# Optimization experiments

Measured on AMD Instinct MI355X. Metric: run time of the kernel, lower is better.

## Reference

```python
import jax, jax.numpy as jnp
import numpy as np

D_MODEL = 1024
MAX_NUM_LAYERS = 4


def setup_inputs() -> dict:
    key = jax.random.key(0)
    ks = jax.random.split(key, 8)
    S, B, D, L = 1024, 2, D_MODEL, 3
    w = lambda k: (jax.random.normal(k, (D, D), dtype=jnp.float32) * 0.02)
    return {
        "x": jax.random.normal(ks[0], (S, B, D), dtype=jnp.float32),
        "layer_outputs": jax.random.normal(ks[1], (L, S, B, D), dtype=jnp.float32),
        "Wq": w(ks[2]), "bq": jnp.zeros((D,), jnp.float32),
        "Wk": w(ks[3]), "bk": jnp.zeros((D,), jnp.float32),
        "Wv": w(ks[4]), "bv": jnp.zeros((D,), jnp.float32),
        "Wo": w(ks[5]), "bo": jnp.zeros((D,), jnp.float32),
        "layer_weights": jnp.ones((MAX_NUM_LAYERS + 1,), jnp.float32),
        "num_heads": 16,
    }


def reference(x, layer_outputs, Wq, bq, Wk, bk, Wv, bv, Wo, bo, layer_weights, num_heads):
    # x: [S, B, D]; layer_outputs: [L, S, B, D] (stacked prev layer outputs)
    S, B, D = x.shape
    H = num_heads
    hd = D // H
    scale = hd ** -0.5
    # q from x only: [S, B*H, hd] -> [BH, S, hd]
    q = (x @ Wq.T + bq).reshape(S, B * H, hd).transpose(1, 0, 2)
    # k/v from x and all previous layer outputs (shared K/V projections)
    xs = jnp.concatenate([x[None], layer_outputs], axis=0)          # [Lp1, S, B, D]
    Lp1 = xs.shape[0]
    k = (xs @ Wk.T + bk).reshape(Lp1, S, B * H, hd).transpose(0, 2, 1, 3)  # [Lp1, BH, S, hd]
    v = (xs @ Wv.T + bv).reshape(Lp1, S, B * H, hd).transpose(0, 2, 1, 3)
    # per-layer scores, softmax over the key axis (torch dim=-2 of stacked scores)
    scores = jnp.einsum('bqd,lbkd->lbqk', q, k) * scale             # [Lp1, BH, S, S]
    attn = jax.nn.softmax(scores, axis=-1)
    lw = jax.nn.softmax(layer_weights[:Lp1])                        # [Lp1]
    combined = jnp.einsum('l,lbqk,lbkd->bqd', lw, attn, v)          # [BH, S, hd]
    combined = combined.transpose(1, 0, 2).reshape(S, B, D)
    return combined @ Wo.T + bo
```

## Files before the change

### kernel.cpp

```cpp
#include <hip/hip_runtime.h>
#include <hip/hip_bf16.h>
#include <math.h>

#define S_LEN   1024
#define BATCH   2
#define DMODEL  1024
#define NHEADS  16
#define HDIM    64
#define BHEADS  32
#define LP1     4
#define ROWS_PL 2048

typedef __attribute__((ext_vector_type(8)))  short bf16x8;
typedef __attribute__((ext_vector_type(4)))  float f32x4;
typedef __attribute__((ext_vector_type(16))) float f32x16;

__device__ inline ushort bf16_rne(float a) {
    unsigned u = __float_as_uint(a);
    return (ushort)((u + 0x7FFFu + ((u >> 16) & 1u)) >> 16);
}
__device__ inline float bf16_up(ushort h) { return __uint_as_float(((unsigned)h) << 16); }
__device__ inline void split_bf16(float a, ushort &hi, ushort &lo) {
    hi = bf16_rne(a);
    lo = bf16_rne(a - bf16_up(hi));
}
__device__ inline uint pk_bf16(float a, float b) {
    float2 f; f.x = a; f.y = b;
    __hip_bfloat162 h = __float22bfloat162_rn(f);
    return *reinterpret_cast<uint*>(&h);
}
#if __has_builtin(__builtin_amdgcn_exp2f)
__device__ inline float fast_exp2(float x) { return __builtin_amdgcn_exp2f(x); }
#else
__device__ inline float fast_exp2(float x) { return exp2f(x); }
#endif

__device__ inline void permswap(uint &a, uint &b) {
    asm("v_permlane32_swap_b32 %0, %1" : "+v"(a), "+v"(b));
}

__device__ inline void glds16(const ushort* g, ushort* l) {
    __builtin_amdgcn_global_load_lds(
        (const __attribute__((address_space(1))) void*)g,
        (__attribute__((address_space(3))) void*)l, 16, 0, 0);
}

__device__ inline void wait4_barrier() {
    asm volatile("s_waitcnt vmcnt(4)" ::: "memory");
    __builtin_amdgcn_s_barrier();
    __builtin_amdgcn_sched_barrier(0);
}
__device__ inline void wait0_barrier() {
    asm volatile("s_waitcnt vmcnt(0)" ::: "memory");
    __builtin_amdgcn_s_barrier();
    __builtin_amdgcn_sched_barrier(0);
}

#define SCLF 0.18033688011112042f

__global__ __launch_bounds__(256)
void presplit(const float* __restrict__ x, const float* __restrict__ lo,
              const float* __restrict__ Wq, const float* __restrict__ Wk,
              const float* __restrict__ Wv, const float* __restrict__ Wo,
              ushort* __restrict__ XsH, ushort* __restrict__ WH,
              ushort* __restrict__ WL)
{
    const int bid = blockIdx.x;
    const float* src; ushort* dh; ushort* dl = nullptr; int local;
    if (bid < 1024)      { src = x;  dh = XsH;           local = bid; }
    else if (bid < 4096) { src = lo; dh = XsH + 2097152; local = bid - 1024; }
    else {
        const int z = (bid - 4096) >> 9;
        local = (bid - 4096) & 511;
        const float* wsrc[4] = { Wq, Wk, Wv, Wo };
        src = wsrc[z];
        dh = WH + (size_t)z * 1048576;
        if (z == 0 || z == 3) dl = WL + (size_t)z * 1048576;
    }
    const int i = (local * 256 + threadIdx.x) * 8;
    float v[8];
    *(float4*)&v[0] = *(const float4*)(src + i);
    *(float4*)&v[4] = *(const float4*)(src + i + 4);
    ushort h[8];
    #pragma unroll
    for (int j = 0; j < 8; ++j) h[j] = bf16_rne(v[j]);
    *(uint4*)(dh + i) = *(uint4*)h;
    if (dl) {
        ushort l[8];
        #pragma unroll
        for (int j = 0; j < 8; ++j) l[j] = bf16_rne(v[j] - bf16_up(h[j]));
        *(uint4*)(dl + i) = *(uint4*)l;
    }
}

__global__ __launch_bounds__(256, 2)
void proj_qkv(const ushort* __restrict__ XsH,
              const ushort* __restrict__ WH, const ushort* __restrict__ WL,
              const float* __restrict__ bq, const float* __restrict__ bk,
              const float* __restrict__ bv,
              ushort* __restrict__ qhb, ushort* __restrict__ qlb,
              ushort* __restrict__ kout, ushort* __restrict__ vout)
{
    __shared__ ushort smem[32768];
    const int bid = blockIdx.x;
    const int t   = threadIdx.x;
    const int wv  = t >> 6, lane = t & 63;
    const int quad = lane >> 4, r = lane & 15;
    const int lrow = lane >> 2;
    const int lch  = ((lane & 3) ^ (lrow & 3) ^ ((lrow >> 2) & 3)) * 8;
    const int q0x  = ((quad ^ (r & 3) ^ ((r >> 2) & 3)) << 3);
    const int cn   = lane & 15;

    if (bid >= 512) {
        const int fid = bid - 512;
        const int xcd = fid & 7, idx = fid >> 3;
        const int mt  = xcd * 2 + (idx >> 4);
        const int nt  = idx & 15;
        const int m0 = mt * 128, n0 = nt * 64;

        const int wm = wv & 1, wn = wv >> 1;
        const int mBase = wm * 64, nBase = wn * 32;

        const ushort* Asrc0 = XsH + (size_t)(m0 + wv * 16 + lrow) * DMODEL + lch;
        const ushort* Asrc1 = Asrc0 + (size_t)64 * DMODEL;
        const ushort* Bhsrc = WH  + (size_t)(n0 + wv * 16 + lrow) * DMODEL + lch;
        const ushort* Blsrc = WL  + (size_t)(n0 + wv * 16 + lrow) * DMODEL + lch;

        f32x4 acc[4][2];
        #pragma unroll
        for (int i = 0; i < 4; ++i)
            #pragma unroll
            for (int j = 0; j < 2; ++j) acc[i][j] = (f32x4){0.f, 0.f, 0.f, 0.f};

        #pragma unroll
        for (int s = 0; s < 2; ++s) {
            ushort* sb = smem + s * 8192;
            const int off = s * 32;
            glds16(Asrc0 + off, sb        + wv * 512);
            glds16(Asrc1 + off, sb + 2048 + wv * 512);
            glds16(Bhsrc + off, sb + 4096 + wv * 512);
            glds16(Blsrc + off, sb + 6144 + wv * 512);
        }

        for (int k = 0; k < 32; ++k) {
            if (k < 31) wait4_barrier(); else wait0_barrier();
            if (k + 2 < 32) {
                ushort* sb = smem + ((k + 2) % 3) * 8192;
                const int off = (k + 2) * 32;
                glds16(Asrc0 + off, sb        + wv * 512);
                glds16(Asrc1 + off, sb + 2048 + wv * 512);
                glds16(Bhsrc + off, sb + 4096 + wv * 512);
                glds16(Blsrc + off, sb + 6144 + wv * 512);
            }
            const ushort* Ah = smem + (k % 3) * 8192;
            const ushort* Bh = Ah + 4096;
            const ushort* Bl = Ah + 6144;
            bf16x8 fa[4], fbh[2], fbl[2];
            #pragma unroll
            for (int i = 0; i < 4; ++i)
                fa[i] = *(const bf16x8*)&Ah[(mBase + i * 16 + r) * 32 + q0x];
            #pragma unroll
            for (int j = 0; j < 2; ++j) {
                fbh[j] = *(const bf16x8*)&Bh[(nBase + j * 16 + r) * 32 + q0x];
                fbl[j] = *(const bf16x8*)&Bl[(nBase + j * 16 + r) * 32 + q0x];
            }
            #pragma unroll
            for (int i = 0; i < 4; ++i)
                #pragma unroll
                for (int j = 0; j < 2; ++j) {
                    acc[i][j] = __builtin_amdgcn_mfma_f32_16x16x32_bf16(fa[i], fbh[j], acc[i][j], 0, 0, 0);
                    acc[i][j] = __builtin_amdgcn_mfma_f32_16x16x32_bf16(fa[i], fbl[j], acc[i][j], 0, 0, 0);
                }
        }

        #pragma unroll
        for (int j = 0; j < 2; ++j) {
            const int n = n0 + nBase + j * 16 + cn;
            const float bvv = bq[n];
            #pragma unroll
            for (int i = 0; i < 4; ++i) {
                const int mrow = m0 + mBase + i * 16 + quad * 4;
                #pragma unroll
                for (int g = 0; g < 4; ++g) {
                    const int m = mrow + g;
                    const float val = (acc[i][j][g] + bvv) * SCLF;
                    const int s = m >> 1, b = m & 1;
                    const int bh = b * 16 + (n >> 6), e = n & 63;
                    const size_t idx2 = (((size_t)bh * S_LEN) + s) * HDIM + e;
                    ushort hi, lov; split_bf16(val, hi, lov);
                    qhb[idx2] = hi; qlb[idx2] = lov;
                }
            }
        }
    } else {
        const int xcd = bid & 7, idx = bid >> 3;
        const int mt  = xcd * 8 + (idx >> 3);
        const int nt  = idx & 7;
        const int m0 = mt * 128, n0 = nt * 128;
        const int lyr = m0 >> 11;

        const int wm = wv & 1, wn = wv >> 1;
        const int mBase = wm * 64, nBase = wn * 64;

        const ushort* KWh = WH + 1048576;
        const ushort* VWh = WH + 2097152;
        const ushort* Asrc0 = XsH + (size_t)(m0 + wv * 16 + lrow) * DMODEL + lch;
        const ushort* Asrc1 = Asrc0 + (size_t)64 * DMODEL;
        const ushort* Bw[2] = { KWh, VWh };
        const ushort* Bsrc[2][2];
        #pragma unroll
        for (int p = 0; p < 2; ++p)
            #pragma unroll
            for (int seg = 0; seg < 2; ++seg)
                Bsrc[p][seg] = Bw[p] + (size_t)(n0 + wv * 32 + seg * 16 + lrow) * DMODEL + lch;

        f32x4 aK[4][4], aV[4][4];
        #pragma unroll
        for (int i = 0; i < 4; ++i)
            #pragma unroll
            for (int j = 0; j < 4; ++j) {
                aK[i][j] = (f32x4){0.f, 0.f, 0.f, 0.f};
                aV[i][j] = (f32x4){0.f, 0.f, 0.f, 0.f};
            }

        {
            ushort* ab = smem;
            glds16(Asrc0, ab        + wv * 512);
            glds16(Asrc1, ab + 2048 + wv * 512);
            #pragma unroll
            for (int s = 0; s < 2; ++s) {
                ushort* bb = smem + 8192 + s * 8192;
                const int off = s * 32;
                #pragma unroll
                for (int p = 0; p < 2; ++p)
                    #pragma unroll
                    for (int seg = 0; seg < 2; ++seg)
                        glds16(Bsrc[p][seg] + off, bb + p * 4096 + (wv * 2 + seg) * 512);
            }
        }

        for (int k = 0; k < 32; ++k) {
            if (k < 31) wait4_barrier(); else wait0_barrier();
            if (k + 1 < 32) {
                ushort* ab = smem + ((k + 1) & 1) * 4096;
                const int off = (k + 1) * 32;
                glds16(Asrc0 + off, ab        + wv * 512);
                glds16(Asrc1 + off, ab + 2048 + wv * 512);
            }
            if (k + 2 < 32) {
                ushort* bb = smem + 8192 + ((k + 2) % 3) * 8192;
                const int off = (k + 2) * 32;
                #pragma unroll
                for (int p = 0; p < 2; ++p)
                    #pragma unroll
                    for (int seg = 0; seg < 2; ++seg)
                        glds16(Bsrc[p][seg] + off, bb + p * 4096 + (wv * 2 + seg) * 512);
            }
            const ushort* Ah = smem + (k & 1) * 4096;
            const ushort* Bb = smem + 8192 + (k % 3) * 8192;

            bf16x8 fa[4];
            #pragma unroll
            for (int i = 0; i < 4; ++i)
                fa[i] = *(const bf16x8*)&Ah[(mBase + i * 16 + r) * 32 + q0x];
            #pragma unroll
            for (int j = 0; j < 4; ++j) {
                const int off2 = (nBase + j * 16 + r) * 32 + q0x;
                const bf16x8 fkh = *(const bf16x8*)&Bb[off2];
                const bf16x8 fvh = *(const bf16x8*)&Bb[4096 + off2];
                #pragma unroll
                for (int i = 0; i < 4; ++i) {
                    aK[i][j] = __builtin_amdgcn_mfma_f32_16x16x32_bf16(fa[i], fkh, aK[i][j], 0, 0, 0);
                    aV[i][j] = __builtin_amdgcn_mfma_f32_16x16x32_bf16(fa[i], fvh, aV[i][j], 0, 0, 0);
                }
            }
        }

        #pragma unroll
        for (int j = 0; j < 4; ++j) {
            const int n = n0 + nBase + j * 16 + cn;
            const float bb = bk[n];
            const int e    = n & 63;
            const int es_k = e >> 4, half_k = (e >> 3) & 1, j_k = e & 7;
            const int h    = n >> 6;
            #pragma unroll
            for (int i = 0; i < 4; ++i) {
                #pragma unroll
                for (int g = 0; g < 4; ++g) {
                    const int m = m0 + mBase + i * 16 + quad * 4 + g;
                    const int rem = m & 2047, s = rem >> 1, b = rem & 1;
                    const int bhI = lyr * 32 + b * 16 + h;
                    const int kt  = s >> 5;
                    const int lnk = half_k * 32 + (s & 31);
                    kout[(size_t)bhI * 65536 + (size_t)(kt * 4 + es_k) * 512 + lnk * 8 + j_k]
                        = bf16_rne(aK[i][j][g] + bb);
                }
            }
        }

        ushort* T = smem;
        __syncthreads();
        #pragma unroll
        for (int j = 0; j < 4; ++j) {
            const int nloc = nBase + j * 16 + cn;
            const float bb = bv[n0 + nloc];
            #pragma unroll
            for (int i = 0; i < 4; ++i) {
                #pragma unroll
                for (int g = 0; g < 4; ++g) {
                    const int mloc = mBase + i * 16 + quad * 4 + g;
                    T[nloc * 130 + mloc] = bf16_rne(aV[i][j][g] + bb);
                }
            }
        }
        __syncthreads();
        {
            const int nloc = t >> 1, bsel = t & 1;
            const int n = n0 + nloc, h = n >> 6;
            const int e = n & 63;
            const int dg = e >> 5, lid_v = e & 31;
            const int s0g = (m0 & 2047) >> 1;
            const int kt0 = s0g >> 5;
            const int bhI = lyr * 32 + bsel * 16 + h;
            #pragma unroll
            for (int c = 0; c < 8; ++c) {
                ushort tmp[8];
                #pragma unroll
                for (int j = 0; j < 8; ++j)
                    tmp[j] = T[nloc * 130 + 2 * (c * 8 + j) + bsel];
                const int kt = kt0 + (c >> 2);
                const int c2 = c & 3;
                const int ks = c2 >> 1, hv = c2 & 1;
                ushort* dstb = vout + (size_t)bhI * 65536 + (size_t)kt * 2048;
                *(uint4*)(dstb + (ks * 2 + dg) * 512 + (hv * 32 + lid_v) * 8) = *(uint4*)tmp;
            }
        }
    }
}

__global__ __launch_bounds__(256)
void proj_o(const ushort* __restrict__ Abf,
            const ushort* __restrict__ Bhg, const ushort* __restrict__ Blg,
            const float* __restrict__ bias, float* __restrict__ outf)
{
    __shared__ ushort smem[3][8192];

    const int fid = blockIdx.x;
    const int xcd = fid & 7, idx = fid >> 3;
    const int mt  = xcd * 2 + (idx >> 4);
    const int nt  = idx & 15;
    const int m0 = mt * 128, n0 = nt * 64;

    const int t  = threadIdx.x;
    const int wv = t >> 6, lane = t & 63;
    const int quad = lane >> 4, r = lane & 15;
    const int wm = wv & 1, wn = wv >> 1;
    const int mBase = wm * 64, nBase = wn * 32;

    const int lrow = lane >> 2;
    const int lch  = ((lane & 3) ^ (lrow & 3) ^ ((lrow >> 2) & 3)) * 8;
    const ushort* Asrc0 = Abf + (size_t)(m0 + wv * 16 + lrow) * DMODEL + lch;
    const ushort* Asrc1 = Asrc0 + (size_t)64 * DMODEL;
    const ushort* Bhsrc = Bhg + (size_t)(n0 + wv * 16 + lrow) * DMODEL + lch;
    const ushort* Blsrc = Blg + (size_t)(n0 + wv * 16 + lrow) * DMODEL + lch;

    const int q0x = ((quad ^ (r & 3) ^ ((r >> 2) & 3)) << 3);
    f32x4 acc[4][2];
    #pragma unroll
    for (int i = 0; i < 4; ++i)
        #pragma unroll
        for (int j = 0; j < 2; ++j) acc[i][j] = (f32x4){0.f, 0.f, 0.f, 0.f};

    #pragma unroll
    for (int s = 0; s < 2; ++s) {
        ushort* sb = smem[s];
        const int off = s * 32;
        glds16(Asrc0 + off, sb        + wv * 512);
        glds16(Asrc1 + off, sb + 2048 + wv * 512);
        glds16(Bhsrc + off, sb + 4096 + wv * 512);
        glds16(Blsrc + off, sb + 6144 + wv * 512);
    }

    for (int k = 0; k < 32; ++k) {
        if (k < 31) wait4_barrier(); else wait0_barrier();
        if (k + 2 < 32) {
            ushort* sb = smem[(k + 2) % 3];
            const int off = (k + 2) * 32;
            glds16(Asrc0 + off, sb        + wv * 512);
            glds16(Asrc1 + off, sb + 2048 + wv * 512);
            glds16(Bhsrc + off, sb + 4096 + wv * 512);
            glds16(Blsrc + off, sb + 6144 + wv * 512);
        }
        const ushort* Ah = smem[k % 3];
        const ushort* Bh = Ah + 4096;
        const ushort* Bl = Ah + 6144;
        bf16x8 fa[4], fbh[2], fbl[2];
        #pragma unroll
        for (int i = 0; i < 4; ++i)
            fa[i] = *(const bf16x8*)&Ah[(mBase + i * 16 + r) * 32 + q0x];
        #pragma unroll
        for (int j = 0; j < 2; ++j) {
            fbh[j] = *(const bf16x8*)&Bh[(nBase + j * 16 + r) * 32 + q0x];
            fbl[j] = *(const bf16x8*)&Bl[(nBase + j * 16 + r) * 32 + q0x];
        }
        #pragma unroll
        for (int i = 0; i < 4; ++i)
            #pragma unroll
            for (int j = 0; j < 2; ++j) {
                acc[i][j] = __builtin_amdgcn_mfma_f32_16x16x32_bf16(fa[i], fbh[j], acc[i][j], 0, 0, 0);
                acc[i][j] = __builtin_amdgcn_mfma_f32_16x16x32_bf16(fa[i], fbl[j], acc[i][j], 0, 0, 0);
            }
    }

    const int cn = lane & 15;
    #pragma unroll
    for (int j = 0; j < 2; ++j) {
        const int n = n0 + nBase + j * 16 + cn;
        const float bvv = bias[n];
        #pragma unroll
        for (int i = 0; i < 4; ++i) {
            const int mrow = m0 + mBase + i * 16 + quad * 4;
            #pragma unroll
            for (int g = 0; g < 4; ++g)
                outf[(size_t)(mrow + g) * DMODEL + n] = acc[i][j][g] + bvv;
        }
    }
}

__global__ __launch_bounds__(256, 2)
void attn_mfma(const ushort* __restrict__ qhg, const ushort* __restrict__ qlg,
               const ushort* __restrict__ kh, const ushort* __restrict__ vth,
               const float* __restrict__ lwraw, float* __restrict__ part)
{
    const int t    = threadIdx.x;
    const int wv   = t >> 6, lane = t & 63;
    const int half = lane >> 5, lid = lane & 31;

    const int fid  = blockIdx.x;
    const int xcd  = fid & 7, slot = fid >> 3;
    const int pair = xcd * 16 + (slot >> 2);
    const int qt   = slot & 3;
    const int bh   = pair & 31, l = pair >> 5;
    const int qbase = qt * 256 + wv * 64;

    float wl;
    {
        float v[LP1], wm = -3.0e38f;
        #pragma unroll
        for (int i = 0; i < LP1; ++i) { v[i] = lwraw[i]; wm = fmaxf(wm, v[i]); }
        float ws = 0.f;
        #pragma unroll
        for (int i = 0; i < LP1; ++i) { v[i] = __expf(v[i] - wm); ws += v[i]; }
        wl = v[l] / ws;
    }

    bf16x8 qh[2][4], ql[2][4];
    #pragma unroll
    for (int u = 0; u < 2; ++u) {
        const size_t qoff = ((size_t)bh * S_LEN + qbase + u * 32 + lid) * HDIM + half * 8;
        #pragma unroll
        for (int es = 0; es < 4; ++es) {
            qh[u][es] = *(const bf16x8*)(qhg + qoff + es * 16);
            ql[u][es] = *(const bf16x8*)(qlg + qoff + es * 16);
        }
    }

    f32x16 o[2][2];
    #pragma unroll
    for (int u = 0; u < 2; ++u)
        #pragma unroll
        for (int dg = 0; dg < 2; ++dg)
            #pragma unroll
            for (int i = 0; i < 16; ++i) o[u][dg][i] = 0.f;
    float ls[2] = {0.f, 0.f};

    f32x16 zf;
    #pragma unroll
    for (int i = 0; i < 16; ++i) zf[i] = 0.f;

    const size_t kvo = (size_t)(l * BHEADS + bh) * S_LEN * HDIM;
    const ushort* kfb = kh  + kvo + (size_t)lane * 8;
    const ushort* vfb = vth + kvo + (size_t)lane * 8;

    bf16x8 kb[4], kn[4];
    #pragma unroll
    for (int es = 0; es < 4; ++es)
        kb[es] = *(const bf16x8*)(kfb + es * 512);
    #pragma unroll
    for (int es = 0; es < 4; ++es)
        kn[es] = *(const bf16x8*)(kfb + 2048 + es * 512);

    f32x16 sa[2];
    #pragma unroll
    for (int es = 0; es < 4; ++es)
        #pragma unroll
        for (int u = 0; u < 2; ++u) {
            sa[u] = __builtin_amdgcn_mfma_f32_32x32x16_bf16(kb[es], qh[u][es],
                                                            es == 0 ? zf : sa[u], 0, 0, 0);
            sa[u] = __builtin_amdgcn_mfma_f32_32x32x16_bf16(kb[es], ql[u][es], sa[u], 0, 0, 0);
        }

    for (int kt = 0; kt < 32; ++kt) {
        bf16x8 vb[2][2];
        {
            const ushort* vp = vfb + (size_t)kt * 2048;
            #pragma unroll
            for (int ks = 0; ks < 2; ++ks)
                #pragma unroll
                for (int dg = 0; dg < 2; ++dg)
                    vb[ks][dg] = *(const bf16x8*)(vp + (ks * 2 + dg) * 512);
        }

        bf16x8 pf[2][2];
        #pragma unroll
        for (int ks = 0; ks < 2; ++ks) {
            #pragma unroll
            for (int u = 0; u < 2; ++u) {
                const float p0 = fast_exp2(sa[u][8 * ks + 0]);
                const float p1 = fast_exp2(sa[u][8 * ks + 1]);
                const float p2 = fast_exp2(sa[u][8 * ks + 2]);
                const float p3 = fast_exp2(sa[u][8 * ks + 3]);
                const float p4 = fast_exp2(sa[u][8 * ks + 4]);
                const float p5 = fast_exp2(sa[u][8 * ks + 5]);
                const float p6 = fast_exp2(sa[u][8 * ks + 6]);
                const float p7 = fast_exp2(sa[u][8 * ks + 7]);
                ls[u] += ((p0 + p1) + (p2 + p3)) + ((p4 + p5) + (p6 + p7));

                uint a0 = pk_bf16(p0, p1);
                uint a1 = pk_bf16(p2, p3);
                uint b0 = pk_bf16(p4, p5);
                uint b1 = pk_bf16(p6, p7);
                permswap(a0, b0);
                permswap(a1, b1);
                union { uint w[4]; bf16x8 v; } pu;
                pu.w[0] = a0; pu.w[1] = a1; pu.w[2] = b0; pu.w[3] = b1;
                pf[ks][u] = pu.v;
            }
        }

        #pragma unroll
        for (int es = 0; es < 4; ++es) kb[es] = kn[es];
        {
            const ushort* kp = kfb + (size_t)((kt + 2) & 31) * 2048;
            #pragma unroll
            for (int es = 0; es < 4; ++es) kn[es] = *(const bf16x8*)(kp + es * 512);
        }

        __builtin_amdgcn_s_setprio(1);
        #pragma unroll
        for (int es = 0; es < 4; ++es)
            #pragma unroll
            for (int u = 0; u < 2; ++u) {
                sa[u] = __builtin_amdgcn_mfma_f32_32x32x16_bf16(kb[es], qh[u][es],
                                                                es == 0 ? zf : sa[u], 0, 0, 0);
                sa[u] = __builtin_amdgcn_mfma_f32_32x32x16_bf16(kb[es], ql[u][es], sa[u], 0, 0, 0);
            }
        __builtin_amdgcn_s_setprio(0);

        __builtin_amdgcn_s_setprio(1);
        #pragma unroll
        for (int ks = 0; ks < 2; ++ks)
            #pragma unroll
            for (int dg = 0; dg < 2; ++dg)
                #pragma unroll
                for (int u = 0; u < 2; ++u)
                    o[u][dg] = __builtin_amdgcn_mfma_f32_32x32x16_bf16(vb[ks][dg], pf[ks][u], o[u][dg], 0, 0, 0);
        __builtin_amdgcn_s_setprio(0);
    }

    const int b = bh >> 4, hh = bh & 15;
    #pragma unroll
    for (int u = 0; u < 2; ++u) {
        float lsv = ls[u];
        lsv += __shfl_xor(lsv, 32);
        const float sc = wl / lsv;
        const int q = qbase + u * 32 + lid;
        float* pb = part + (size_t)l * (ROWS_PL * DMODEL)
                  + ((size_t)q * BATCH + b) * DMODEL + hh * HDIM;
        #pragma unroll
        for (int dg = 0; dg < 2; ++dg)
            #pragma unroll
            for (int rq = 0; rq < 4; ++rq) {
                float4 vv;
                vv.x = o[u][dg][rq * 4 + 0] * sc;
                vv.y = o[u][dg][rq * 4 + 1] * sc;
                vv.z = o[u][dg][rq * 4 + 2] * sc;
                vv.w = o[u][dg][rq * 4 + 3] * sc;
                *(float4*)(pb + dg * 32 + rq * 8 + half * 4) = vv;
            }
    }
}

__global__ __launch_bounds__(256)
void sum_y(const float* __restrict__ part, ushort* __restrict__ YH)
{
    const int i = (blockIdx.x * 256 + threadIdx.x) * 8;
    float acc[8];
    #pragma unroll
    for (int c = 0; c < 2; ++c) {
        float4 s = *(const float4*)(part + i + c * 4);
        #pragma unroll
        for (int l = 1; l < LP1; ++l) {
            const float4 p = *(const float4*)(part + (size_t)l * 2097152 + i + c * 4);
            s.x += p.x; s.y += p.y; s.z += p.z; s.w += p.w;
        }
        acc[c * 4 + 0] = s.x; acc[c * 4 + 1] = s.y;
        acc[c * 4 + 2] = s.z; acc[c * 4 + 3] = s.w;
    }
    uint out[4];
    #pragma unroll
    for (int c = 0; c < 4; ++c) out[c] = pk_bf16(acc[c * 2], acc[c * 2 + 1]);
    *(uint4*)(YH + i) = *(uint4*)out;
}

extern "C" void kernel_launch(void* const* d_in, const int* in_sizes, int n_in,
                              void* d_out, int out_size, void* d_ws, size_t ws_size,
                              hipStream_t stream) {
    const float* x  = (const float*)d_in[0];
    const float* lo = (const float*)d_in[1];
    const float* Wq = (const float*)d_in[2];
    const float* bq = (const float*)d_in[3];
    const float* Wk = (const float*)d_in[4];
    const float* bk = (const float*)d_in[5];
    const float* Wv = (const float*)d_in[6];
    const float* bv = (const float*)d_in[7];
    const float* Wo = (const float*)d_in[8];
    const float* bo = (const float*)d_in[9];
    const float* lw = (const float*)d_in[10];
    float* out = (float*)d_out;

    char* ws = (char*)d_ws;
    ushort* XsH  = (ushort*)(ws);
    ushort* WH   = (ushort*)(ws + 16777216);
    ushort* WL   = (ushort*)(ws + 25165824);
    ushort* qhb  = (ushort*)(ws + 33554432);
    ushort* qlb  = (ushort*)(ws + 37748736);
    ushort* khb  = (ushort*)(ws + 41943040);
    ushort* vthb = (ushort*)(ws + 58720256);
    float*  part = (float*)(ws + 75497472);
    ushort* YH   = (ushort*)(ws + 109051904);

    dim3 blk(256);
    presplit<<<dim3(6144), blk, 0, stream>>>(x, lo, Wq, Wk, Wv, Wo, XsH, WH, WL);
    proj_qkv<<<dim3(768), blk, 0, stream>>>(XsH, WH, WL, bq, bk, bv,
                                            qhb, qlb, khb, vthb);
    attn_mfma<<<dim3(512), blk, 0, stream>>>(qhb, qlb, khb, vthb, lw, part);
    sum_y<<<dim3(1024), blk, 0, stream>>>(part, YH);
    proj_o<<<dim3(256), blk, 0, stream>>>(YH, WH + 3145728, WL + 3145728, bo, out);
}
```

Before: 231.8 us.

## Fuse per-layer partial sum into output projection A-tile loading

Removes the separate sum_y kernel and has the output projection read the four fp32 per-layer partial buffers directly. It sums and converts them to bf16 in registers before writing the A tile to shared memory. The B-tile pipeline shrinks from triple to double buffering, with register prefetch of the next A chunk overlapping the MFMA work. This drops one launch and the bf16 intermediate round trip. In exchange each proj_o block rereads 4x fp32 A data (16 column tiles share the same rows), which adds global traffic and register pressure.

```diff
diff --git a/kernel.cpp b/kernel.cpp
--- a/kernel.cpp
+++ b/kernel.cpp
@@ -339,11 +339,11 @@
 }
 
 __global__ __launch_bounds__(256)
-void proj_o(const ushort* __restrict__ Abf,
-            const ushort* __restrict__ Bhg, const ushort* __restrict__ Blg,
-            const float* __restrict__ bias, float* __restrict__ outf)
+void proj_oy(const float* __restrict__ part,
+             const ushort* __restrict__ Bhg, const ushort* __restrict__ Blg,
+             const float* __restrict__ bias, float* __restrict__ outf)
 {
-    __shared__ ushort smem[3][8192];
+    __shared__ ushort smem[2][8192];
 
     const int fid = blockIdx.x;
     const int xcd = fid & 7, idx = fid >> 3;
@@ -359,10 +359,12 @@
 
     const int lrow = lane >> 2;
     const int lch  = ((lane & 3) ^ (lrow & 3) ^ ((lrow >> 2) & 3)) * 8;
-    const ushort* Asrc0 = Abf + (size_t)(m0 + wv * 16 + lrow) * DMODEL + lch;
-    const ushort* Asrc1 = Asrc0 + (size_t)64 * DMODEL;
+    const float* Ap0 = part + (size_t)(m0 + wv * 16 + lrow) * DMODEL + lch;
+    const float* Ap1 = Ap0 + (size_t)64 * DMODEL;
     const ushort* Bhsrc = Bhg + (size_t)(n0 + wv * 16 + lrow) * DMODEL + lch;
     const ushort* Blsrc = Blg + (size_t)(n0 + wv * 16 + lrow) * DMODEL + lch;
+    const int aoff0 = wv * 512 + lane * 8;
+    const int aoff1 = 2048 + wv * 512 + lane * 8;
 
     const int q0x = ((quad ^ (r & 3) ^ ((r >> 2) & 3)) << 3);
     f32x4 acc[4][2];
@@ -371,27 +373,50 @@
         #pragma unroll
         for (int j = 0; j < 2; ++j) acc[i][j] = (f32x4){0.f, 0.f, 0.f, 0.f};
 
-    #pragma unroll
-    for (int s = 0; s < 2; ++s) {
-        ushort* sb = smem[s];
-        const int off = s * 32;
-        glds16(Asrc0 + off, sb        + wv * 512);
-        glds16(Asrc1 + off, sb + 2048 + wv * 512);
-        glds16(Bhsrc + off, sb + 4096 + wv * 512);
-        glds16(Blsrc + off, sb + 6144 + wv * 512);
+    auto sum_cvt = [&](const float* ap, uint4* outv) {
+        float4 s0 = *(const float4*)(ap);
+        float4 s1 = *(const float4*)(ap + 4);
+        #pragma unroll
+        for (int l = 1; l < LP1; ++l) {
+            const float4 p0 = *(const float4*)(ap + (size_t)l * 2097152);
+            const float4 p1 = *(const float4*)(ap + (size_t)l * 2097152 + 4);
+            s0.x += p0.x; s0.y += p0.y; s0.z += p0.z; s0.w += p0.w;
+            s1.x += p1.x; s1.y += p1.y; s1.z += p1.z; s1.w += p1.w;
+        }
+        ushort h[8];
+        h[0] = bf16_rne(s0.x); h[1] = bf16_rne(s0.y);
+        h[2] = bf16_rne(s0.z); h[3] = bf16_rne(s0.w);
+        h[4] = bf16_rne(s1.x); h[5] = bf16_rne(s1.y);
+        h[6] = bf16_rne(s1.z); h[7] = bf16_rne(s1.w);
+        *outv = *(const uint4*)h;
+    };
+
+    {
+        uint4 a0, a1;
+        sum_cvt(Ap0, &a0);
+        sum_cvt(Ap1, &a1);
+        glds16(Bhsrc, smem[0] + 4096 + wv * 512);
+        glds16(Blsrc, smem[0] + 6144 + wv * 512);
+        *(uint4*)&smem[0][aoff0] = a0;
+        *(uint4*)&smem[0][aoff1] = a1;
     }
 
     for (int k = 0; k < 32; ++k) {
-        if (k < 31) wait4_barrier(); else wait0_barrier();
-        if (k + 2 < 32) {
-            ushort* sb = smem[(k + 2) % 3];
-            const int off = (k + 2) * 32;
-            glds16(Asrc0 + off, sb        + wv * 512);
-            glds16(Asrc1 + off, sb + 2048 + wv * 512);
-            glds16(Bhsrc + off, sb + 4096 + wv * 512);
-            glds16(Blsrc + off, sb + 6144 + wv * 512);
-        }
-        const ushort* Ah = smem[k % 3];
+        __syncthreads();
+        float4 ar[2][LP1][2];
+        if (k + 1 < 32) {
+            const int off = (k + 1) * 32;
+            #pragma unroll
+            for (int l = 0; l < LP1; ++l) {
+                ar[0][l][0] = *(const float4*)(Ap0 + (size_t)l * 2097152 + off);
+                ar[0][l][1] = *(const float4*)(Ap0 + (size_t)l * 2097152 + off + 4);
+                ar[1][l][0] = *(const float4*)(Ap1 + (size_t)l * 2097152 + off);
+                ar[1][l][1] = *(const float4*)(Ap1 + (size_t)l * 2097152 + off + 4);
+            }
+            glds16(Bhsrc + off, smem[(k + 1) & 1] + 4096 + wv * 512);
+            glds16(Blsrc + off, smem[(k + 1) & 1] + 6144 + wv * 512);
+        }
+        const ushort* Ah = smem[k & 1];
         const ushort* Bh = Ah + 4096;
         const ushort* Bl = Ah + 6144;
         bf16x8 fa[4], fbh[2], fbl[2];
@@ -410,6 +435,27 @@
                 acc[i][j] = __builtin_amdgcn_mfma_f32_16x16x32_bf16(fa[i], fbh[j], acc[i][j], 0, 0, 0);
                 acc[i][j] = __builtin_amdgcn_mfma_f32_16x16x32_bf16(fa[i], fbl[j], acc[i][j], 0, 0, 0);
             }
+        if (k + 1 < 32) {
+            ushort* sb = smem[(k + 1) & 1];
+            #pragma unroll
+            for (int st = 0; st < 2; ++st) {
+                float4 s0 = ar[st][0][0];
+                float4 s1 = ar[st][0][1];
+                #pragma unroll
+                for (int l = 1; l < LP1; ++l) {
+                    s0.x += ar[st][l][0].x; s0.y += ar[st][l][0].y;
+                    s0.z += ar[st][l][0].z; s0.w += ar[st][l][0].w;
+                    s1.x += ar[st][l][1].x; s1.y += ar[st][l][1].y;
+                    s1.z += ar[st][l][1].z; s1.w += ar[st][l][1].w;
+                }
+                ushort h[8];
+                h[0] = bf16_rne(s0.x); h[1] = bf16_rne(s0.y);
+                h[2] = bf16_rne(s0.z); h[3] = bf16_rne(s0.w);
+                h[4] = bf16_rne(s1.x); h[5] = bf16_rne(s1.y);
+                h[6] = bf16_rne(s1.z); h[7] = bf16_rne(s1.w);
+                *(uint4*)&sb[st ? aoff1 : aoff0] = *(const uint4*)h;
+            }
+        }
     }
 
     const int cn = lane & 15;
@@ -589,28 +635,6 @@
                 *(float4*)(pb + dg * 32 + rq * 8 + half * 4) = vv;
             }
     }
-}
-
-__global__ __launch_bounds__(256)
-void sum_y(const float* __restrict__ part, ushort* __restrict__ YH)
-{
-    const int i = (blockIdx.x * 256 + threadIdx.x) * 8;
-    float acc[8];
-    #pragma unroll
-    for (int c = 0; c < 2; ++c) {
-        float4 s = *(const float4*)(part + i + c * 4);
-        #pragma unroll
-        for (int l = 1; l < LP1; ++l) {
-            const float4 p = *(const float4*)(part + (size_t)l * 2097152 + i + c * 4);
-            s.x += p.x; s.y += p.y; s.z += p.z; s.w += p.w;
-        }
-        acc[c * 4 + 0] = s.x; acc[c * 4 + 1] = s.y;
-        acc[c * 4 + 2] = s.z; acc[c * 4 + 3] = s.w;
-    }
-    uint out[4];
-    #pragma unroll
-    for (int c = 0; c < 4; ++c) out[c] = pk_bf16(acc[c * 2], acc[c * 2 + 1]);
-    *(uint4*)(YH + i) = *(uint4*)out;
 }
 
 extern "C" void kernel_launch(void* const* d_in, const int* in_sizes, int n_in,
@@ -638,13 +662,11 @@
     ushort* khb  = (ushort*)(ws + 41943040);
     ushort* vthb = (ushort*)(ws + 58720256);
     float*  part = (float*)(ws + 75497472);
-    ushort* YH   = (ushort*)(ws + 109051904);
 
     dim3 blk(256);
     presplit<<<dim3(6144), blk, 0, stream>>>(x, lo, Wq, Wk, Wv, Wo, XsH, WH, WL);
     proj_qkv<<<dim3(768), blk, 0, stream>>>(XsH, WH, WL, bq, bk, bv,
                                             qhb, qlb, khb, vthb);
     attn_mfma<<<dim3(512), blk, 0, stream>>>(qhb, qlb, khb, vthb, lw, part);
-    sum_y<<<dim3(1024), blk, 0, stream>>>(part, YH);
-    proj_o<<<dim3(256), blk, 0, stream>>>(YH, WH + 3145728, WL + 3145728, bo, out);
-}
+    proj_oy<<<dim3(256), blk, 0, stream>>>(part, WH + 3145728, WL + 3145728, bo, out);
+}
```

New measurement: 259.0 us. 1.12x slower.
